# Kernel optimization log

Hardware: AMD Instinct MI355X
Metric: run time of the kernel (lower is better)

Reference implementation:

```python
import jax, jax.numpy as jnp
import numpy as np

DIM = 768
B, N = 8, 2048


def setup_inputs() -> dict:
    key = jax.random.key(0)
    k = jax.random.split(key, 8)
    s = 1.0 / np.sqrt(DIM)
    return {
        "x": jax.random.normal(k[0], (B, N, DIM), jnp.float32),
        "x2": jax.random.normal(k[1], (B, N, DIM), jnp.float32),
        "x3": jax.random.normal(k[2], (B, N, DIM), jnp.float32),
        "W1": jax.random.uniform(k[3], (DIM, DIM), jnp.float32, -s, s),
        "b1": jax.random.uniform(k[4], (DIM,), jnp.float32, -s, s),
        "W2": jax.random.uniform(k[5], (DIM, DIM), jnp.float32, -s, s),
        "b2": jax.random.uniform(k[6], (DIM,), jnp.float32, -s, s),
        "w": jnp.ones((1,), jnp.float32),
    }


def _cross_attention(x, x2, W, b):
    # key = softmax(x2.transpose(1,2), dim=1) -> softmax over feature axis, then [B, D, N]
    key = jnp.swapaxes(jax.nn.softmax(x2, axis=-1), 1, 2)  # [B, D, N]
    query = jax.nn.softmax(x2, axis=1)                      # [B, N, D], softmax over tokens
    context = jnp.einsum('bnd,bdm->bnm', x, key)            # [B, N, N]
    atten = jnp.einsum('bnm,bmd->bnd', context, query)      # [B, N, D]
    return atten @ W.T + b


def reference(x, x2, x3, W1, b1, W2, b2, w):
    a1 = _cross_attention(x, x2, W1, b1)
    a2 = _cross_attention(x, x3, W2, b2)
    f = jax.nn.sigmoid(w)  # scalar gate, broadcast
    atten = a1 * f + a2 * f
    return atten + x
```

## Files before the change

### kernel.cpp

```cpp
#include <hip/hip_runtime.h>

#define DIMD 768
#define NTOK 2048
#define NB   8

typedef __attribute__((ext_vector_type(8))) short bfrag8;
typedef __attribute__((ext_vector_type(4))) float accf4;

__device__ __forceinline__ unsigned short f2bf(float f) {
  unsigned u = __float_as_uint(f);
  return (unsigned short)((u + 0x7fffu + ((u >> 16) & 1u)) >> 16);
}

__device__ __forceinline__ void glds16(const void* g, void* l) {
  __builtin_amdgcn_global_load_lds(
      (const __attribute__((address_space(1))) void*)g,
      (__attribute__((address_space(3))) void*)l, 16, 0, 0);
}


__device__ __forceinline__ void packw_body(int blk, const float* __restrict__ W1,
                                           const float* __restrict__ W2,
                                           unsigned short* __restrict__ Wcat) {
  int gid = blk * 256 + threadIdx.x;
  int r = gid / 192, c4 = (gid % 192) * 4;
  float4 a = *(const float4*)(W1 + (size_t)r * DIMD + c4);
  float4 b = *(const float4*)(W2 + (size_t)r * DIMD + c4);
  union { unsigned short us[4]; uint2 u2; } ra, rb;
  ra.us[0] = f2bf(a.x); ra.us[1] = f2bf(a.y); ra.us[2] = f2bf(a.z); ra.us[3] = f2bf(a.w);
  rb.us[0] = f2bf(b.x); rb.us[1] = f2bf(b.y); rb.us[2] = f2bf(b.z); rb.us[3] = f2bf(b.w);
  *(uint2*)(Wcat + (size_t)r * 1536 + c4) = ra.u2;
  *(uint2*)(Wcat + (size_t)r * 1536 + 768 + c4) = rb.u2;
}

__device__ __forceinline__ void packx_body(int blk, const float* __restrict__ x,
                                           unsigned short* __restrict__ xb) {
  size_t gid = (size_t)blk * 256 + threadIdx.x;
  const float4* x4 = (const float4*)x;
  float4 v0 = x4[gid * 2], v1 = x4[gid * 2 + 1];
  union { unsigned short us[8]; uint4 u4; } r;
  r.us[0] = f2bf(v0.x); r.us[1] = f2bf(v0.y); r.us[2] = f2bf(v0.z); r.us[3] = f2bf(v0.w);
  r.us[4] = f2bf(v1.x); r.us[5] = f2bf(v1.y); r.us[6] = f2bf(v1.z); r.us[7] = f2bf(v1.w);
  ((uint4*)xb)[gid] = r.u4;
}

template <int TMD, int TND, int EPI>
__device__ __forceinline__ void gemm_body(
    unsigned short* As, unsigned short* Bs, int bid,
    const unsigned short* __restrict__ A, const unsigned short* __restrict__ B,
    void* __restrict__ Cout, int K, int lda, int ldb, int ldc, int ntx,
    long long sA, long long sB, long long sC,
    const float* __restrict__ wg, const float* __restrict__ b1v,
    const float* __restrict__ b2v, const float* __restrict__ xres) {
  constexpr int TM = 64 * TMD, TN = 64 * TND;
  constexpr int ASZ = TM * 64, BSZ = TN * 64;
  __shared__ float csi[64 * TND];
  const int t = threadIdx.x, w = t >> 6, lane = t & 63;
  const int bz = bid & 7;
  const int r = bid >> 3;
  const int by = r / ntx, bx = r - by * ntx;
  const int m0 = by * TM, n0 = bx * TN;
  const unsigned short* Ab = A + (size_t)bz * sA;
  const unsigned short* Bb = B + (size_t)bz * sB;
  const int srow = lane >> 3;
  const int scol = (((lane & 7) ^ (lane >> 3)) * 8);

  auto stage = [&](int buf, int k0) {
    unsigned short* Ad = As + buf * ASZ;
    unsigned short* Bd = Bs + buf * BSZ;
#pragma unroll
    for (int l = 0; l < 2 * TND; ++l) {
      int chunk = l * 4 + w;
      int row = chunk * 8 + srow;
      glds16(Bb + (size_t)(n0 + row) * ldb + k0 + scol,
             (char*)Bd + chunk * 1024 + lane * 16);
    }
#pragma unroll
    for (int l = 0; l < 2 * TMD; ++l) {
      int chunk = l * 4 + w;
      int row = chunk * 8 + srow;
      glds16(Ab + (size_t)(m0 + row) * lda + k0 + scol,
             (char*)Ad + chunk * 1024 + lane * 16);
    }
  };

  stage(0, 0);

  if (EPI == 2) {
    for (int c = t; c < TN; c += 256) {
      const float* cp = b1v + (size_t)bz * 64 * DIMD + n0 + c;
      float s = 0.f;
#pragma unroll
      for (int p = 0; p < 64; ++p) s += cp[(size_t)p * DIMD];
      csi[c] = 1.0f / s;
    }
  }

  accf4 zero = {0.f, 0.f, 0.f, 0.f};
  accf4 acc[2 * TMD][2 * TND];
#pragma unroll
  for (int i = 0; i < 2 * TMD; ++i)
#pragma unroll
    for (int j = 0; j < 2 * TND; ++j) acc[i][j] = zero;

  const int wm = (w & 1) * (32 * TMD), wn = (w >> 1) * (32 * TND);
  const int lm = lane & 15, qd = lane >> 4;
  const int lsw = (lm & 7) << 3;

  __syncthreads();

  const int nt = K / 64;
  int cur = 0;
#pragma unroll 2
  for (int tt = 0; tt < nt; ++tt) {
    if (tt + 1 < nt) stage(cur ^ 1, (tt + 1) * 64);
    const unsigned short* Ar = As + cur * ASZ;
    const unsigned short* Br = Bs + cur * BSZ;
#pragma unroll
    for (int kc = 0; kc < 2; ++kc) {
      bfrag8 av[2 * TMD], bv[2 * TND];
      const int kslot = (((kc << 2) | qd) << 3) ^ lsw;
#pragma unroll
      for (int i = 0; i < 2 * TMD; ++i)
        av[i] = *(const bfrag8*)(Ar + (wm + i * 16 + lm) * 64 + kslot);
#pragma unroll
      for (int j = 0; j < 2 * TND; ++j)
        bv[j] = *(const bfrag8*)(Br + (wn + j * 16 + lm) * 64 + kslot);
      __builtin_amdgcn_s_setprio(1);
#pragma unroll
      for (int i = 0; i < 2 * TMD; ++i)
#pragma unroll
        for (int j = 0; j < 2 * TND; ++j)
          acc[i][j] = __builtin_amdgcn_mfma_f32_16x16x32_bf16(av[i], bv[j], acc[i][j], 0, 0, 0);
      __builtin_amdgcn_s_setprio(0);
    }
    if (tt + 1 < nt) {
      asm volatile("s_waitcnt vmcnt(0)\n\ts_barrier" ::: "memory");
    }
    cur ^= 1;
  }

  if (EPI == 0) {
    unsigned short* Cb = (unsigned short*)Cout + (size_t)bz * sC;
#pragma unroll
    for (int i = 0; i < 2 * TMD; ++i)
#pragma unroll
      for (int j = 0; j < 2 * TND; ++j) {
        int col = n0 + wn + j * 16 + lm;
#pragma unroll
        for (int rr = 0; rr < 4; ++rr) {
          int row = m0 + wm + i * 16 + qd * 4 + rr;
          Cb[(size_t)row * ldc + col] = f2bf(acc[i][j][rr]);
        }
      }
  } else if (EPI == 1) {
    float gate = 1.f / (1.f + __expf(-wg[0]));
    float* Co = (float*)Cout + (size_t)bz * sC;
    const float* Xr = xres + (size_t)bz * sC;
#pragma unroll
    for (int j = 0; j < 2 * TND; ++j) {
      int col = n0 + wn + j * 16 + lm;
      float gb = gate * (b1v[col] + b2v[col]);
#pragma unroll
      for (int i = 0; i < 2 * TMD; ++i)
#pragma unroll
        for (int rr = 0; rr < 4; ++rr) {
          int row = m0 + wm + i * 16 + qd * 4 + rr;
          size_t idx = (size_t)row * ldc + col;
          Co[idx] = gate * acc[i][j][rr] + gb + Xr[idx];
        }
    }
  } else {
    unsigned short* Cb = (unsigned short*)Cout + (size_t)bz * sC;
#pragma unroll
    for (int j = 0; j < 2 * TND; ++j) {
      int lc = wn + j * 16 + lm;
      int col = n0 + lc;
      float ci = csi[lc];
#pragma unroll
      for (int i = 0; i < 2 * TMD; ++i)
#pragma unroll
        for (int rr = 0; rr < 4; ++rr) {
          int row = m0 + wm + i * 16 + qd * 4 + rr;
          Cb[(size_t)row * ldc + col] = f2bf(acc[i][j][rr] * ci);
        }
    }
  }
}

__global__ __launch_bounds__(256) void rowcol_kernel(
    const float* __restrict__ x2, const float* __restrict__ x3,
    float* __restrict__ csp1, float* __restrict__ csp2,
    float* __restrict__ rsf,
    const float* __restrict__ W1, const float* __restrict__ W2,
    unsigned short* __restrict__ Wcat, int npw) {
  int blk = blockIdx.x;
  if (blk >= 1024) {
    if (blk < 1024 + npw) packw_body(blk - 1024, W1, W2, Wcat);
    return;
  }
  const int sel = blk >> 9, b = (blk >> 6) & 7, tile = blk & 63;
  const float* xin = sel ? x3 : x2;
  float* csp = sel ? csp2 : csp1;
  float* rso = rsf + (size_t)sel * NB * NTOK + (size_t)b * NTOK + tile * 32;
  const float* xb_ = xin + ((size_t)b * NTOK + tile * 32) * DIMD;
  const int t = threadIdx.x, w = t >> 6, lane = t & 63;
  __shared__ float cred[4][DIMD];

  const int d0 = lane * 12;
  float cs[12];
#pragma unroll
  for (int i = 0; i < 12; ++i) cs[i] = 0.f;

#pragma unroll
  for (int v = 0; v < 8; ++v) {
    int tok = w * 8 + v;
    const float* row = xb_ + (size_t)tok * DIMD + d0;
    float4 a = *(const float4*)(row);
    float4 c = *(const float4*)(row + 4);
    float4 d = *(const float4*)(row + 8);
    float e[12];
    e[0] = __expf(a.x); e[1] = __expf(a.y); e[2] = __expf(a.z); e[3] = __expf(a.w);
    e[4] = __expf(c.x); e[5] = __expf(c.y); e[6] = __expf(c.z); e[7] = __expf(c.w);
    e[8] = __expf(d.x); e[9] = __expf(d.y); e[10] = __expf(d.z); e[11] = __expf(d.w);
    float rp = 0.f;
#pragma unroll
    for (int i = 0; i < 12; ++i) { rp += e[i]; cs[i] += e[i]; }
#pragma unroll
    for (int off = 32; off; off >>= 1) rp += __shfl_xor(rp, off, 64);
    if (lane == 0) rso[tok] = sqrtf(1.0f / rp);
  }
#pragma unroll
  for (int i = 0; i < 12; ++i) cred[w][d0 + i] = cs[i];
  __syncthreads();
#pragma unroll
  for (int i = 0; i < 3; ++i) {
    int d = t * 3 + i;
    float s = cred[0][d] + cred[1][d] + cred[2][d] + cred[3][d];
    csp[((size_t)b * 64 + tile) * DIMD + d] = s;
  }
}

__global__ __launch_bounds__(256) void ft_kernel(
    const float* __restrict__ x2, const float* __restrict__ x3,
    const float* __restrict__ rsf,
    unsigned short* __restrict__ Ft1, unsigned short* __restrict__ Ft2) {
  __shared__ __align__(16) unsigned short etile[192 * 72];
  const int blk = blockIdx.x;
  const int sel = blk >> 10, lb = blk & 1023;
  const int b = lb >> 7, rr = lb & 127, ntile = rr >> 2, dc = rr & 3;
  const float* xin = sel ? x3 : x2;
  unsigned short* Ft = sel ? Ft2 : Ft1;
  const float* rsv = rsf + (size_t)sel * NB * NTOK + (size_t)b * NTOK + ntile * 64;
  const int t = threadIdx.x;

  const int tok = t >> 2, q4 = t & 3;
  const float* row = xin + ((size_t)b * NTOK + ntile * 64 + tok) * DIMD + dc * 192 + q4 * 48;
  const float fsc = rsv[tok];
#pragma unroll
  for (int j = 0; j < 12; ++j) {
    float4 v = *(const float4*)(row + j * 4);
    int dl = q4 * 48 + j * 4;
    etile[(dl + 0) * 72 + tok] = f2bf(__expf(v.x) * fsc);
    etile[(dl + 1) * 72 + tok] = f2bf(__expf(v.y) * fsc);
    etile[(dl + 2) * 72 + tok] = f2bf(__expf(v.z) * fsc);
    etile[(dl + 3) * 72 + tok] = f2bf(__expf(v.w) * fsc);
  }
  __syncthreads();
#pragma unroll
  for (int k = 0; k < 6; ++k) {
    int dl = (t >> 3) + k * 32;
    int g = t & 7;
    uint4 e8 = *(const uint4*)(etile + dl * 72 + g * 8);
    *(uint4*)(Ft + ((size_t)b * DIMD + dc * 192 + dl) * NTOK + ntile * 64 + g * 8) = e8;
  }
}

template <int TMD, int TND, int EPI>
__global__ __launch_bounds__(256) void mfma_bt(
    const unsigned short* __restrict__ A, const unsigned short* __restrict__ B,
    void* __restrict__ Cout, int K, int lda, int ldb, int ldc, int ntx,
    long long sA, long long sB, long long sC,
    const float* __restrict__ wg, const float* __restrict__ b1v,
    const float* __restrict__ b2v, const float* __restrict__ xres) {
  __shared__ __align__(16) unsigned short As[2 * 64 * TMD * 64];
  __shared__ __align__(16) unsigned short Bs[2 * 64 * TND * 64];
  gemm_body<TMD, TND, EPI>(As, Bs, blockIdx.x, A, B, Cout, K, lda, ldb, ldc, ntx,
                           sA, sB, sC, wg, b1v, b2v, xres);
}

__global__ __launch_bounds__(256) void sgemm_s(
    const unsigned short* __restrict__ Ft1, const float* __restrict__ csp1,
    const unsigned short* __restrict__ Ft2, const float* __restrict__ csp2,
    unsigned short* __restrict__ Ca, unsigned short* __restrict__ Cb) {
  __shared__ __align__(16) unsigned short As[2 * 128 * 64];
  __shared__ __align__(16) unsigned short Bs[2 * 128 * 64];
  bool second = blockIdx.x >= 288;
  const unsigned short* F = second ? Ft2 : Ft1;
  const float* csp = second ? csp2 : csp1;
  unsigned short* C = second ? Cb : Ca;
  int blk = second ? (blockIdx.x - 288) : blockIdx.x;
  gemm_body<2, 2, 2>(As, Bs, blk, F, F, C, NTOK, NTOK, NTOK, 1536, 6,
                     768LL * NTOK, 768LL * NTOK, 768LL * 1536,
                     nullptr, csp, nullptr, nullptr);
}

__global__ __launch_bounds__(256) void s2_packx_kernel(
    const unsigned short* __restrict__ Wcat, const unsigned short* __restrict__ Scat,
    unsigned short* __restrict__ Bt, const float* __restrict__ x,
    unsigned short* __restrict__ xb) {
  __shared__ __align__(16) unsigned short As[2 * 128 * 64];
  __shared__ __align__(16) unsigned short Bs[2 * 128 * 64];
  int blk = blockIdx.x;
  if (blk < 288) {
    gemm_body<2, 2, 0>(As, Bs, blk, Wcat, Scat, Bt, 1536, 1536, 1536, 768, 6,
                       0LL, 768LL * 1536, 768LL * 768,
                       nullptr, nullptr, nullptr, nullptr);
  } else {
    packx_body(blk - 288, x, xb);
  }
}

extern "C" void kernel_launch(void* const* d_in, const int* in_sizes, int n_in,
                              void* d_out, int out_size, void* d_ws, size_t ws_size,
                              hipStream_t stream) {
  const float* x  = (const float*)d_in[0];
  const float* x2 = (const float*)d_in[1];
  const float* x3 = (const float*)d_in[2];
  const float* W1 = (const float*)d_in[3];
  const float* b1 = (const float*)d_in[4];
  const float* W2 = (const float*)d_in[5];
  const float* b2 = (const float*)d_in[6];
  const float* w  = (const float*)d_in[7];
  float* out = (float*)d_out;
  char* ws = (char*)d_ws;

  unsigned short* Ft1  = (unsigned short*)(ws + 0);
  unsigned short* Ft2  = (unsigned short*)(ws + 25165824);
  unsigned short* Scat = (unsigned short*)(ws + 50331648);
  unsigned short* Wcat = (unsigned short*)(ws + 69206016);
  float* csp1 = (float*)(ws + 71565312);
  float* csp2 = (float*)(ws + 73138176);
  float* rsf  = (float*)(ws + 74711040);
  unsigned short* Bt = (unsigned short*)(ws + 0);
  unsigned short* xb = (unsigned short*)(ws + 9437184);

  dim3 blk(256);

  rowcol_kernel<<<1600, blk, 0, stream>>>(x2, x3, csp1, csp2, rsf, W1, W2, Wcat, 576);
  ft_kernel<<<2048, blk, 0, stream>>>(x2, x3, rsf, Ft1, Ft2);
  sgemm_s<<<576, blk, 0, stream>>>(Ft1, csp1, Ft2, csp2, Scat, Scat + 768);
  s2_packx_kernel<<<6432, blk, 0, stream>>>(Wcat, Scat, Bt, x, xb);
  mfma_bt<2, 2, 1><<<768, blk, 0, stream>>>(xb, Bt, out, DIMD, DIMD, DIMD, DIMD, 6,
                                            (long long)NTOK * DIMD, 768LL * 768,
                                            (long long)NTOK * DIMD, w, b1, b2, x);
}
```

Baseline: 328.0 us.

## Exploit symmetry of Ft·Ftᵀ Gram matrix, computing only upper-triangular tiles

The per-batch D×D product Ft·Ftᵀ is a symmetric Gram matrix, so sgemm_s now launches only the 21 triangular 128×128 tiles per batch and matrix instead of all 36. Off-diagonal tiles write their transposed mirror through an LDS staging buffer. The column-scale reciprocal is now computed once per (batch, d) in extra ft_kernel blocks rather than redundantly inside every gemm block. The costs are an extra LDS transpose pass with barriers in the epilogue and a small serial tile-index decode loop.

```diff
diff --git a/kernel.cpp b/kernel.cpp
--- a/kernel.cpp
+++ b/kernel.cpp
@@ -55,6 +55,7 @@
   constexpr int TM = 64 * TMD, TN = 64 * TND;
   constexpr int ASZ = TM * 64, BSZ = TN * 64;
   __shared__ float csi[64 * TND];
+  __shared__ float csir[64 * TMD];
   const int t = threadIdx.x, w = t >> 6, lane = t & 63;
   const int bz = bid & 7;
   const int r = bid >> 3;
@@ -87,13 +88,8 @@
   stage(0, 0);
 
   if (EPI == 2) {
-    for (int c = t; c < TN; c += 256) {
-      const float* cp = b1v + (size_t)bz * 64 * DIMD + n0 + c;
-      float s = 0.f;
-#pragma unroll
-      for (int p = 0; p < 64; ++p) s += cp[(size_t)p * DIMD];
-      csi[c] = 1.0f / s;
-    }
+    for (int c = t; c < TN; c += 256) csi[c] = b1v[(size_t)bz * DIMD + n0 + c];
+    for (int c = t; c < TM; c += 256) csir[c] = b1v[(size_t)bz * DIMD + m0 + c];
   }
 
   accf4 zero = {0.f, 0.f, 0.f, 0.f};
@@ -184,6 +180,32 @@
           int row = m0 + wm + i * 16 + qd * 4 + rr;
           Cb[(size_t)row * ldc + col] = f2bf(acc[i][j][rr] * ci);
         }
+    }
+    if (m0 != n0) {
+      unsigned short* mir = As;
+      __syncthreads();
+#pragma unroll
+      for (int i = 0; i < 2 * TMD; ++i) {
+        int lr0 = wm + i * 16 + qd * 4;
+#pragma unroll
+        for (int j = 0; j < 2 * TND; ++j) {
+          int lc = wn + j * 16 + lm;
+          int sw = (lc & 7) << 4;
+          union { unsigned short us[4]; uint2 u2; } p;
+#pragma unroll
+          for (int rr = 0; rr < 4; ++rr)
+            p.us[rr] = f2bf(acc[i][j][rr] * csir[lr0 + rr]);
+          *(uint2*)&mir[lc * 128 + ((lr0) ^ sw)] = p.u2;
+        }
+      }
+      __syncthreads();
+      int e = t >> 1;
+#pragma unroll
+      for (int k = 0; k < 8; ++k) {
+        int d0 = (((t & 1) << 3) + k) << 3;
+        uint4 v = *(const uint4*)&mir[e * 128 + (d0 ^ ((e & 7) << 4))];
+        *(uint4*)&Cb[(size_t)(n0 + e) * ldc + m0 + d0] = v;
+      }
     }
   }
 }
@@ -244,9 +266,23 @@
 __global__ __launch_bounds__(256) void ft_kernel(
     const float* __restrict__ x2, const float* __restrict__ x3,
     const float* __restrict__ rsf,
-    unsigned short* __restrict__ Ft1, unsigned short* __restrict__ Ft2) {
+    unsigned short* __restrict__ Ft1, unsigned short* __restrict__ Ft2,
+    const float* __restrict__ csp1, const float* __restrict__ csp2,
+    float* __restrict__ civ1, float* __restrict__ civ2) {
+  const int blk = blockIdx.x;
+  if (blk >= 2048) {
+    int idx = (blk - 2048) * 256 + threadIdx.x;
+    int sel = idx / 6144, rem = idx - sel * 6144;
+    int b = rem / DIMD, d = rem - b * DIMD;
+    const float* csp = sel ? csp2 : csp1;
+    float s = 0.f;
+    const float* p = csp + (size_t)b * 64 * DIMD + d;
+#pragma unroll 8
+    for (int q = 0; q < 64; ++q) s += p[(size_t)q * DIMD];
+    (sel ? civ2 : civ1)[rem] = 1.0f / s;
+    return;
+  }
   __shared__ __align__(16) unsigned short etile[192 * 72];
-  const int blk = blockIdx.x;
   const int sel = blk >> 10, lb = blk & 1023;
   const int b = lb >> 7, rr = lb & 127, ntile = rr >> 2, dc = rr & 3;
   const float* xin = sel ? x3 : x2;
@@ -290,19 +326,25 @@
 }
 
 __global__ __launch_bounds__(256) void sgemm_s(
-    const unsigned short* __restrict__ Ft1, const float* __restrict__ csp1,
-    const unsigned short* __restrict__ Ft2, const float* __restrict__ csp2,
+    const unsigned short* __restrict__ Ft1, const float* __restrict__ civ1,
+    const unsigned short* __restrict__ Ft2, const float* __restrict__ civ2,
     unsigned short* __restrict__ Ca, unsigned short* __restrict__ Cb) {
   __shared__ __align__(16) unsigned short As[2 * 128 * 64];
   __shared__ __align__(16) unsigned short Bs[2 * 128 * 64];
-  bool second = blockIdx.x >= 288;
+  int bid = blockIdx.x;
+  int bz = bid & 7, r = bid >> 3;
+  bool second = r >= 21;
+  int tri = second ? r - 21 : r;
+  int by = 0;
+  while ((by + 1) * (by + 2) / 2 <= tri) ++by;
+  int bx = tri - by * (by + 1) / 2;
   const unsigned short* F = second ? Ft2 : Ft1;
-  const float* csp = second ? csp2 : csp1;
+  const float* civ = second ? civ2 : civ1;
   unsigned short* C = second ? Cb : Ca;
-  int blk = second ? (blockIdx.x - 288) : blockIdx.x;
-  gemm_body<2, 2, 2>(As, Bs, blk, F, F, C, NTOK, NTOK, NTOK, 1536, 6,
+  int enc = ((by * 6 + bx) << 3) | bz;
+  gemm_body<2, 2, 2>(As, Bs, enc, F, F, C, NTOK, NTOK, NTOK, 1536, 6,
                      768LL * NTOK, 768LL * NTOK, 768LL * 1536,
-                     nullptr, csp, nullptr, nullptr);
+                     nullptr, civ, nullptr, nullptr);
 }
 
 __global__ __launch_bounds__(256) void s2_packx_kernel(
@@ -342,14 +384,16 @@
   float* csp1 = (float*)(ws + 71565312);
   float* csp2 = (float*)(ws + 73138176);
   float* rsf  = (float*)(ws + 74711040);
+  float* civ1 = (float*)(ws + 74842112);
+  float* civ2 = (float*)(ws + 74866688);
   unsigned short* Bt = (unsigned short*)(ws + 0);
   unsigned short* xb = (unsigned short*)(ws + 9437184);
 
   dim3 blk(256);
 
   rowcol_kernel<<<1600, blk, 0, stream>>>(x2, x3, csp1, csp2, rsf, W1, W2, Wcat, 576);
-  ft_kernel<<<2048, blk, 0, stream>>>(x2, x3, rsf, Ft1, Ft2);
-  sgemm_s<<<576, blk, 0, stream>>>(Ft1, csp1, Ft2, csp2, Scat, Scat + 768);
+  ft_kernel<<<2096, blk, 0, stream>>>(x2, x3, rsf, Ft1, Ft2, csp1, csp2, civ1, civ2);
+  sgemm_s<<<336, blk, 0, stream>>>(Ft1, civ1, Ft2, civ2, Scat, Scat + 768);
   s2_packx_kernel<<<6432, blk, 0, stream>>>(Wcat, Scat, Bt, x, xb);
   mfma_bt<2, 2, 1><<<768, blk, 0, stream>>>(xb, Bt, out, DIMD, DIMD, DIMD, DIMD, 6,
                                             (long long)NTOK * DIMD, 768LL * 768,
```

New measurement: 308.8 us. 1.06x faster.
